# Kernel tuning notes

Hardware: AMD Instinct MI355X
Metric: run time of the kernel (lower is better)

Reference implementation:

```python
import jax, jax.numpy as jnp
import numpy as np
from jax.experimental.ode import odeint

LATENT, HIDDEN, OUT, BATCH, T = 128, 256, 128, 4096, 100
DEC_H = 64  # MLPDecoder default hidden_dim


def setup_inputs() -> dict:
    key = jax.random.key(0)
    ks = jax.random.split(key, 8)
    s = lambda k, shp, fan: jax.random.normal(k, shp, jnp.float32) / np.sqrt(fan)
    return {
        "z0": jax.random.normal(ks[0], (BATCH, LATENT), jnp.float32),
        "times": jnp.arange(T, dtype=jnp.float32) * 0.01,  # increasing time grid
        # ode_func: tanh MLP latent->hidden->latent
        "W1": s(ks[1], (LATENT, HIDDEN), LATENT),
        "b1": jnp.zeros((HIDDEN,), jnp.float32),
        "W2": s(ks[2], (HIDDEN, LATENT), HIDDEN),
        "b2": jnp.zeros((LATENT,), jnp.float32),
        # MLPDecoder: latent->64->relu->64->relu->out
        "dW1": s(ks[3], (LATENT, DEC_H), LATENT),
        "db1": jnp.zeros((DEC_H,), jnp.float32),
        "dW2": s(ks[4], (DEC_H, DEC_H), DEC_H),
        "db2": jnp.zeros((DEC_H,), jnp.float32),
        "dW3": s(ks[5], (DEC_H, OUT), DEC_H),
        "db3": jnp.zeros((OUT,), jnp.float32),
    }


def reference(z0, times, W1, b1, W2, b2, dW1, db1, dW2, db2, dW3, db3):
    def ode_func(z, t):  # dz/dt, autonomous tanh-MLP dynamics
        return jnp.tanh(z @ W1 + b1) @ W2 + b2

    # adaptive dopri5 (Dormand-Prince RK45), tolerances match torchdiffeq defaults
    z_traj = odeint(ode_func, z0, times, rtol=1e-7, atol=1e-9)  # [T, B, L]

    h = jax.nn.relu(z_traj @ dW1 + db1)
    h = jax.nn.relu(h @ dW2 + db2)
    y = h @ dW3 + db3                  # [T, B, out]
    return jnp.transpose(y, (1, 0, 2))  # [B, T, out]
```

## Files before the change

kernel.cpp:

```cpp
#include <hip/hip_runtime.h>

#define LATENT 128
#define HIDDEN 256
#define OUTD   128
#define TT     100
#define DECH   64
#define NMACRO 5

typedef _Float16 f16x8 __attribute__((ext_vector_type(8)));
typedef float    f32x4 __attribute__((ext_vector_type(4)));

#define MFMA16(a,b,c) __builtin_amdgcn_mfma_f32_16x16x32_f16((a),(b),(c),0,0,0)

__device__ __forceinline__ float tanh_fast(float x){
    float e = __expf(2.f*x);
    return 1.f - 2.f*__builtin_amdgcn_rcpf(e + 1.f);
}

__device__ __forceinline__ void bar_nodrain(){
    __builtin_amdgcn_sched_barrier(0);
    asm volatile("s_waitcnt lgkmcnt(0)" ::: "memory");
    __builtin_amdgcn_sched_barrier(0);
    __builtin_amdgcn_s_barrier();
    __builtin_amdgcn_sched_barrier(0);
}

__device__ __forceinline__ f16x8 lds_rd8(const _Float16* b, int sB, int row, int colE){
    int off = row*sB + colE*2; off ^= (row&7)<<4;
    return *(const f16x8*)((const char*)b + off);
}
__device__ __forceinline__ void lds_wr1(_Float16* b, int sB, int row, int colE, float v){
    int off = row*sB + colE*2; off ^= (row&7)<<4;
    *(_Float16*)((char*)b + off) = (_Float16)v;
}
__device__ __forceinline__ void lds_wr2(_Float16* b, int sB, int row, int colE, float lo, float hi){
    int off = row*sB + colE*2; off ^= (row&7)<<4;
    union { _Float16 h[2]; unsigned u; } pk;
    pk.h[0] = (_Float16)lo; pk.h[1] = (_Float16)hi;
    *(unsigned*)((char*)b + off) = pk.u;
}

__device__ __forceinline__ f16x8 gbl_bfrag(const float* W, int ldN, int k0, int n){
    f16x8 f;
#pragma unroll
    for(int i=0;i<8;++i) f[i] = (_Float16)W[(size_t)(k0+i)*ldN + n];
    return f;
}
__device__ __forceinline__ f16x8 gbl_bfrag_pk(const float* W, int ldN, int q, int lg, int n){
    f16x8 f;
#pragma unroll
    for(int i=0;i<8;++i){
        int k = 32*q + 4*lg + (i>>1) + 16*(i&1);
        f[i] = (_Float16)W[(size_t)k*ldN + n];
    }
    return f;
}

__global__ __launch_bounds__(512, 2) void ode_decoder_kernel(
    const float* __restrict__ z0, const float* __restrict__ times,
    const float* __restrict__ W1, const float* __restrict__ b1,
    const float* __restrict__ W2, const float* __restrict__ b2,
    const float* __restrict__ dW1, const float* __restrict__ db1,
    const float* __restrict__ dW2, const float* __restrict__ db2,
    const float* __restrict__ dW3, const float* __restrict__ db3,
    float* __restrict__ out)
{
    __shared__ _Float16 z_lds[16*LATENT]  __attribute__((aligned(16)));
    __shared__ _Float16 h_lds[16*HIDDEN]  __attribute__((aligned(16)));
    __shared__ _Float16 epz[16*LATENT]    __attribute__((aligned(16)));
    __shared__ _Float16 epf[16*LATENT]    __attribute__((aligned(16)));
    __shared__ _Float16 h1i[2][64*DECH]   __attribute__((aligned(16)));
    __shared__ _Float16 h2i[2][64*DECH]   __attribute__((aligned(16)));
    __shared__ float    tl[TT];

    const int tid  = threadIdx.x;
    const int wv   = tid >> 6;
    const int lane = tid & 63;
    const int lr   = lane & 15;
    const int lg   = lane >> 4;
    const int row0 = 4*lg;
    const int gRow0 = blockIdx.x * 16;
    const int nsl  = wv & 3;
    const int mtb  = 2*(wv >> 2);
    const int ph   = wv >> 2;

    if(tid < TT) tl[tid] = times[tid];

    f16x8 w1f[2][4];
#pragma unroll
    for(int t=0;t<2;++t)
#pragma unroll
        for(int q=0;q<4;++q)
            w1f[t][q] = gbl_bfrag(W1, HIDDEN, 32*q+8*lg, 32*wv+16*t+lr);
    f16x8 w2f[8];
#pragma unroll
    for(int q=0;q<8;++q)
        w2f[q] = gbl_bfrag_pk(W2, LATENT, q, lg, 16*wv+lr);

    f16x8 dw1f[4], dw2f[2], dw3f[2];
#pragma unroll
    for(int q=0;q<4;++q) dw1f[q] = gbl_bfrag(dW1, DECH, 32*q+8*lg, 16*nsl+lr);
#pragma unroll
    for(int q=0;q<2;++q) dw2f[q] = gbl_bfrag(dW2, DECH, 32*q+8*lg, 16*nsl+lr);
#pragma unroll
    for(int q=0;q<2;++q) dw3f[q] = gbl_bfrag(dW3, OUTD, 32*q+8*lg, 16*wv+lr);

    const float b1v0 = b1[32*wv+lr], b1v1 = b1[32*wv+16+lr];
    const float b2v  = b2[16*wv+lr];
    const float db1v = db1[16*nsl+lr], db2v = db2[16*nsl+lr];
    const float db3v = db3[16*wv+lr];

    f32x4 z, acc = {0,0,0,0};
    f32x4 UA = {0,0,0,0}, VA = {0,0,0,0}, UB = {0,0,0,0}, VB = {0,0,0,0};
#pragma unroll
    for(int r=0;r<4;++r){
        z[r] = z0[(size_t)(gRow0+row0+r)*LATENT + 16*wv + lr];
        lds_wr1(z_lds, LATENT*2, row0+r, 16*wv+lr, z[r]);
    }
    bar_nodrain();

    auto G1SEG = [&]{
        f16x8 az[4];
#pragma unroll
        for(int q=0;q<4;++q) az[q] = lds_rd8(z_lds, LATENT*2, lr, 32*q+8*lg);
        f32x4 c0 = {b1v0,b1v0,b1v0,b1v0};
        f32x4 c1 = {b1v1,b1v1,b1v1,b1v1};
#pragma unroll
        for(int q=0;q<4;++q){ c0 = MFMA16(az[q], w1f[0][q], c0); c1 = MFMA16(az[q], w1f[1][q], c1); }
#pragma unroll
        for(int r=0;r<4;++r)
            lds_wr2(h_lds, HIDDEN*2, row0+r, 2*(16*wv+lr), tanh_fast(c0[r]), tanh_fast(c1[r]));
    };
    auto G2SEG = [&]() -> f32x4 {
        f16x8 ah[8];
#pragma unroll
        for(int q=0;q<8;++q) ah[q] = lds_rd8(h_lds, HIDDEN*2, lr, 32*q+8*lg);
        f32x4 ca = {b2v,b2v,b2v,b2v}, cb = {0,0,0,0};
#pragma unroll
        for(int q=0;q<4;++q){ ca = MFMA16(ah[q], w2f[q], ca); cb = MFMA16(ah[4+q], w2f[4+q], cb); }
        return ca + cb;
    };
    auto WRZ = [&](f32x4 zs){
#pragma unroll
        for(int r=0;r<4;++r) lds_wr1(z_lds, LATENT*2, row0+r, 16*wv+lr, zs[r]);
    };
    auto WREP = [&](f32x4 zz, f32x4 ff){
#pragma unroll
        for(int r=0;r<4;++r){
            lds_wr1(epz, LATENT*2, row0+r, 16*wv+lr, zz[r]);
            lds_wr1(epf, LATENT*2, row0+r, 16*wv+lr, ff[r]);
        }
    };
    auto UVGEMM = [&]{
        f32x4 u = {0,0,0,0}, v = {0,0,0,0};
#pragma unroll
        for(int q=0;q<4;++q){
            u = MFMA16(lds_rd8(epz, LATENT*2, lr, 32*q+8*lg), dw1f[q], u);
            v = MFMA16(lds_rd8(epf, LATENT*2, lr, 32*q+8*lg), dw1f[q], v);
        }
        UB = u; VB = v;
    };
    auto CMB = [&](int par, int p0, int jj){
        const float t0 = tl[20*jj];
        const float tB = (jj==NMACRO-1) ? tl[TT-1] : tl[20*jj+20];
        const float hp = tB - t0, rhp = 1.f/hp;
        _Float16* h1 = h1i[par];
#pragma unroll
        for(int i=0;i<2;++i){
            const int pi = 2*ph + i;
            const float th = (tl[p0+pi]-t0)*rhp;
            const float t2 = th*th, t3 = t2*th;
            const float a0 = 2.f*t3-3.f*t2+1.f, a1 = (t3-2.f*t2+th)*hp;
            const float a2 = 3.f*t2-2.f*t3,     a3 = (t3-t2)*hp;
#pragma unroll
            for(int r=0;r<4;++r){
                float v = a0*UA[r] + a1*VA[r] + a2*UB[r] + a3*VB[r] + db1v;
                lds_wr1(h1, DECH*2, 16*pi+row0+r, 16*nsl+lr, fmaxf(v,0.f));
            }
        }
    };
    auto DG2 = [&](int par){
        const _Float16* h1 = h1i[par];
        _Float16* h2 = h2i[par];
#pragma unroll
        for(int m=0;m<2;++m){ int mt = mtb+m;
            f32x4 c = {db2v,db2v,db2v,db2v};
#pragma unroll
            for(int q=0;q<2;++q) c = MFMA16(lds_rd8(h1, DECH*2, 16*mt+lr, 32*q+8*lg), dw2f[q], c);
#pragma unroll
            for(int r=0;r<4;++r) lds_wr1(h2, DECH*2, 16*mt+row0+r, 16*nsl+lr, fmaxf(c[r],0.f));
        }
    };
    auto DG3 = [&](int par, int p0){
        const _Float16* h2 = h2i[par];
#pragma unroll
        for(int mt=0;mt<4;++mt){
            f32x4 c = {db3v,db3v,db3v,db3v};
#pragma unroll
            for(int q=0;q<2;++q) c = MFMA16(lds_rd8(h2, DECH*2, 16*mt+lr, 32*q+8*lg), dw3f[q], c);
#pragma unroll
            for(int r=0;r<4;++r)
                out[(size_t)(gRow0+row0+r)*TT*OUTD + (size_t)(p0+mt)*OUTD + 16*wv+lr] = c[r];
        }
    };

#pragma unroll 1
    for(int j=0;j<NMACRO;++j){
        const int  m0 = 20*j;
        const int  m1 = (m0+20 < TT-1) ? m0+20 : TT-1;
        const float hj = tl[m1]-tl[m0];
        const bool dA = (j>=1);
        const bool dD = (j>=2);
        const int  rb = 5*(j-1);

        G1SEG(); if(dD){ DG2((rb-1)&1); DG3((rb-2)&1, 4*(rb-2)); }
        bar_nodrain();
        {
            f32x4 k1 = G2SEG();
            WREP(z, k1);
            if(dD) DG3((rb-1)&1, 4*(rb-1));
            acc = z + k1*(hj*(1.f/6.f));
            WRZ(z + k1*(hj*0.5f));
        }
        bar_nodrain();
        G1SEG(); UVGEMM();
        bar_nodrain();
        {
            f32x4 k2 = G2SEG();
            if(dA) CMB(rb&1, 4*rb, j-1);
            acc += k2*(hj*(1.f/3.f));
            WRZ(z + k2*(hj*0.5f));
        }
        bar_nodrain();
        G1SEG(); if(dA){ CMB((rb+1)&1, 4*(rb+1), j-1); DG2(rb&1); }
        bar_nodrain();
        {
            f32x4 k3 = G2SEG();
            if(dA){ CMB((rb+2)&1, 4*(rb+2), j-1); DG2((rb+1)&1); DG3(rb&1, 4*rb); }
            acc += k3*(hj*(1.f/3.f));
            WRZ(z + k3*hj);
        }
        bar_nodrain();
        G1SEG(); if(dA){ CMB((rb+3)&1, 4*(rb+3), j-1); DG2((rb+2)&1); DG3((rb+1)&1, 4*(rb+1)); }
        bar_nodrain();
        {
            f32x4 k4 = G2SEG();
            if(dA){ CMB((rb+4)&1, 4*(rb+4), j-1); DG2((rb+3)&1); DG3((rb+2)&1, 4*(rb+2)); }
            z = acc + k4*(hj*(1.f/6.f));
            WRZ(z);
        }
        UA = UB; VA = VB;
        bar_nodrain();
    }

    {
        G1SEG(); DG2(19&1); DG3(18&1, 72);
        bar_nodrain();
        {
            f32x4 kt = G2SEG();
            WREP(z, kt);
            DG3(19&1, 76);
        }
        bar_nodrain();
        UVGEMM();
        bar_nodrain();
        CMB(20&1, 80, 4);
        bar_nodrain();
        CMB(21&1, 84, 4); DG2(20&1);
        bar_nodrain();
        CMB(22&1, 88, 4); DG2(21&1); DG3(20&1, 80);
        bar_nodrain();
        CMB(23&1, 92, 4); DG2(22&1); DG3(21&1, 84);
        bar_nodrain();
        CMB(24&1, 96, 4); DG2(23&1); DG3(22&1, 88);
        bar_nodrain();
        DG2(24&1); DG3(23&1, 92);
        bar_nodrain();
        DG3(24&1, 96);
    }
}

extern "C" void kernel_launch(void* const* d_in, const int* in_sizes, int n_in,
                              void* d_out, int out_size, void* d_ws, size_t ws_size,
                              hipStream_t stream) {
    ode_decoder_kernel<<<dim3(256), dim3(512), 0, stream>>>(
        (const float*)d_in[0],  (const float*)d_in[1],
        (const float*)d_in[2],  (const float*)d_in[3],
        (const float*)d_in[4],  (const float*)d_in[5],
        (const float*)d_in[6],  (const float*)d_in[7],
        (const float*)d_in[8],  (const float*)d_in[9],
        (const float*)d_in[10], (const float*)d_in[11],
        (float*)d_out);
}
```

Before: 59.40 us.

## Specialize waves into ODE-solver and decoder groups with double-buffered endpoint LDS

```diff
diff --git a/kernel.cpp b/kernel.cpp
--- a/kernel.cpp
+++ b/kernel.cpp
@@ -56,7 +56,7 @@
     return f;
 }
 
-__global__ __launch_bounds__(512, 2) void ode_decoder_kernel(
+__global__ __launch_bounds__(512, 1) void ode_decoder_kernel(
     const float* __restrict__ z0, const float* __restrict__ times,
     const float* __restrict__ W1, const float* __restrict__ b1,
     const float* __restrict__ W2, const float* __restrict__ b2,
@@ -65,12 +65,12 @@
     const float* __restrict__ dW3, const float* __restrict__ db3,
     float* __restrict__ out)
 {
-    __shared__ _Float16 z_lds[16*LATENT]  __attribute__((aligned(16)));
-    __shared__ _Float16 h_lds[16*HIDDEN]  __attribute__((aligned(16)));
-    __shared__ _Float16 epz[16*LATENT]    __attribute__((aligned(16)));
-    __shared__ _Float16 epf[16*LATENT]    __attribute__((aligned(16)));
-    __shared__ _Float16 h1i[2][64*DECH]   __attribute__((aligned(16)));
-    __shared__ _Float16 h2i[2][64*DECH]   __attribute__((aligned(16)));
+    __shared__ _Float16 z_lds[16*LATENT]   __attribute__((aligned(16)));
+    __shared__ _Float16 h_lds[16*HIDDEN]   __attribute__((aligned(16)));
+    __shared__ _Float16 epz[2][16*LATENT]  __attribute__((aligned(16)));
+    __shared__ _Float16 epf[2][16*LATENT]  __attribute__((aligned(16)));
+    __shared__ _Float16 h1i[2][64*DECH]    __attribute__((aligned(16)));
+    __shared__ _Float16 h2i[2][64*DECH]    __attribute__((aligned(16)));
     __shared__ float    tl[TT];
 
     const int tid  = threadIdx.x;
@@ -80,42 +80,55 @@
     const int lg   = lane >> 4;
     const int row0 = 4*lg;
     const int gRow0 = blockIdx.x * 16;
-    const int nsl  = wv & 3;
-    const int mtb  = 2*(wv >> 2);
-    const int ph   = wv >> 2;
+    const bool ct  = (wv < 4);
+    const int wc   = wv & 3;
+    const int dwv  = wv & 3;
+    const int nsl  = dwv;
 
     if(tid < TT) tl[tid] = times[tid];
 
-    f16x8 w1f[2][4];
-#pragma unroll
-    for(int t=0;t<2;++t)
-#pragma unroll
-        for(int q=0;q<4;++q)
-            w1f[t][q] = gbl_bfrag(W1, HIDDEN, 32*q+8*lg, 32*wv+16*t+lr);
-    f16x8 w2f[8];
-#pragma unroll
-    for(int q=0;q<8;++q)
-        w2f[q] = gbl_bfrag_pk(W2, LATENT, q, lg, 16*wv+lr);
-
-    f16x8 dw1f[4], dw2f[2], dw3f[2];
-#pragma unroll
-    for(int q=0;q<4;++q) dw1f[q] = gbl_bfrag(dW1, DECH, 32*q+8*lg, 16*nsl+lr);
-#pragma unroll
-    for(int q=0;q<2;++q) dw2f[q] = gbl_bfrag(dW2, DECH, 32*q+8*lg, 16*nsl+lr);
-#pragma unroll
-    for(int q=0;q<2;++q) dw3f[q] = gbl_bfrag(dW3, OUTD, 32*q+8*lg, 16*wv+lr);
-
-    const float b1v0 = b1[32*wv+lr], b1v1 = b1[32*wv+16+lr];
-    const float b2v  = b2[16*wv+lr];
-    const float db1v = db1[16*nsl+lr], db2v = db2[16*nsl+lr];
-    const float db3v = db3[16*wv+lr];
-
-    f32x4 z, acc = {0,0,0,0};
+    f16x8 w1f[4][4], w2f[2][8];
+    f32x4 z[2], acc[2];
+    float b1v[4], b2v[2];
+    f16x8 dw1f[4], dw2f[2], dw3f[2][2];
     f32x4 UA = {0,0,0,0}, VA = {0,0,0,0}, UB = {0,0,0,0}, VB = {0,0,0,0};
-#pragma unroll
-    for(int r=0;r<4;++r){
-        z[r] = z0[(size_t)(gRow0+row0+r)*LATENT + 16*wv + lr];
-        lds_wr1(z_lds, LATENT*2, row0+r, 16*wv+lr, z[r]);
+    float db1v = 0.f, db2v = 0.f, db3v[2] = {0.f,0.f};
+
+    if(ct){
+#pragma unroll
+        for(int t=0;t<4;++t)
+#pragma unroll
+            for(int q=0;q<4;++q)
+                w1f[t][q] = gbl_bfrag(W1, HIDDEN, 32*q+8*lg, 64*wc+16*t+lr);
+#pragma unroll
+        for(int u=0;u<2;++u)
+#pragma unroll
+            for(int q=0;q<8;++q)
+                w2f[u][q] = gbl_bfrag_pk(W2, LATENT, q, lg, 32*wc+16*u+lr);
+#pragma unroll
+        for(int t=0;t<4;++t) b1v[t] = b1[64*wc+16*t+lr];
+#pragma unroll
+        for(int u=0;u<2;++u) b2v[u] = b2[32*wc+16*u+lr];
+#pragma unroll
+        for(int u=0;u<2;++u)
+#pragma unroll
+            for(int r=0;r<4;++r){
+                z[u][r] = z0[(size_t)(gRow0+row0+r)*LATENT + 32*wc+16*u+lr];
+                lds_wr1(z_lds, LATENT*2, row0+r, 32*wc+16*u+lr, z[u][r]);
+            }
+    } else {
+#pragma unroll
+        for(int q=0;q<4;++q) dw1f[q] = gbl_bfrag(dW1, DECH, 32*q+8*lg, 16*nsl+lr);
+#pragma unroll
+        for(int q=0;q<2;++q) dw2f[q] = gbl_bfrag(dW2, DECH, 32*q+8*lg, 16*nsl+lr);
+#pragma unroll
+        for(int u=0;u<2;++u)
+#pragma unroll
+            for(int q=0;q<2;++q)
+                dw3f[u][q] = gbl_bfrag(dW3, OUTD, 32*q+8*lg, 32*dwv+16*u+lr);
+        db1v = db1[16*nsl+lr]; db2v = db2[16*nsl+lr];
+#pragma unroll
+        for(int u=0;u<2;++u) db3v[u] = db3[32*dwv+16*u+lr];
     }
     bar_nodrain();
 
@@ -123,40 +136,58 @@
         f16x8 az[4];
 #pragma unroll
         for(int q=0;q<4;++q) az[q] = lds_rd8(z_lds, LATENT*2, lr, 32*q+8*lg);
-        f32x4 c0 = {b1v0,b1v0,b1v0,b1v0};
-        f32x4 c1 = {b1v1,b1v1,b1v1,b1v1};
-#pragma unroll
-        for(int q=0;q<4;++q){ c0 = MFMA16(az[q], w1f[0][q], c0); c1 = MFMA16(az[q], w1f[1][q], c1); }
-#pragma unroll
-        for(int r=0;r<4;++r)
-            lds_wr2(h_lds, HIDDEN*2, row0+r, 2*(16*wv+lr), tanh_fast(c0[r]), tanh_fast(c1[r]));
-    };
-    auto G2SEG = [&]() -> f32x4 {
+        f32x4 c[4];
+#pragma unroll
+        for(int t=0;t<4;++t) c[t] = (f32x4){b1v[t],b1v[t],b1v[t],b1v[t]};
+#pragma unroll
+        for(int q=0;q<4;++q)
+#pragma unroll
+            for(int t=0;t<4;++t) c[t] = MFMA16(az[q], w1f[t][q], c[t]);
+#pragma unroll
+        for(int m=0;m<2;++m){
+            const int uu = 2*wc+m;
+#pragma unroll
+            for(int r=0;r<4;++r)
+                lds_wr2(h_lds, HIDDEN*2, row0+r, 2*(16*uu+lr),
+                        tanh_fast(c[2*m][r]), tanh_fast(c[2*m+1][r]));
+        }
+    };
+    auto G2SEG = [&](f32x4 kk[2]){
         f16x8 ah[8];
 #pragma unroll
         for(int q=0;q<8;++q) ah[q] = lds_rd8(h_lds, HIDDEN*2, lr, 32*q+8*lg);
-        f32x4 ca = {b2v,b2v,b2v,b2v}, cb = {0,0,0,0};
-#pragma unroll
-        for(int q=0;q<4;++q){ ca = MFMA16(ah[q], w2f[q], ca); cb = MFMA16(ah[4+q], w2f[4+q], cb); }
-        return ca + cb;
-    };
-    auto WRZ = [&](f32x4 zs){
-#pragma unroll
-        for(int r=0;r<4;++r) lds_wr1(z_lds, LATENT*2, row0+r, 16*wv+lr, zs[r]);
-    };
-    auto WREP = [&](f32x4 zz, f32x4 ff){
+#pragma unroll
+        for(int u=0;u<2;++u){
+            f32x4 ca = (f32x4){b2v[u],b2v[u],b2v[u],b2v[u]};
+            f32x4 cb = (f32x4){0,0,0,0};
+#pragma unroll
+            for(int q=0;q<4;++q){ ca = MFMA16(ah[q], w2f[u][q], ca); cb = MFMA16(ah[4+q], w2f[u][4+q], cb); }
+            kk[u] = ca + cb;
+        }
+    };
+    auto WRZ = [&](f32x4 zs0, f32x4 zs1){
 #pragma unroll
         for(int r=0;r<4;++r){
-            lds_wr1(epz, LATENT*2, row0+r, 16*wv+lr, zz[r]);
-            lds_wr1(epf, LATENT*2, row0+r, 16*wv+lr, ff[r]);
-        }
-    };
-    auto UVGEMM = [&]{
+            lds_wr1(z_lds, LATENT*2, row0+r, 32*wc+lr,    zs0[r]);
+            lds_wr1(z_lds, LATENT*2, row0+r, 32*wc+16+lr, zs1[r]);
+        }
+    };
+    auto WREP = [&](int par, f32x4 kk[2]){
+#pragma unroll
+        for(int u=0;u<2;++u)
+#pragma unroll
+            for(int r=0;r<4;++r){
+                lds_wr1(epz[par], LATENT*2, row0+r, 32*wc+16*u+lr, z[u][r]);
+                lds_wr1(epf[par], LATENT*2, row0+r, 32*wc+16*u+lr, kk[u][r]);
+            }
+    };
+
+    auto UVGEMM = [&](int par){
         f32x4 u = {0,0,0,0}, v = {0,0,0,0};
 #pragma unroll
         for(int q=0;q<4;++q){
-            u = MFMA16(lds_rd8(epz, LATENT*2, lr, 32*q+8*lg), dw1f[q], u);
-            v = MFMA16(lds_rd8(epf, LATENT*2, lr, 32*q+8*lg), dw1f[q], v);
+            u = MFMA16(lds_rd8(epz[par], LATENT*2, lr, 32*q+8*lg), dw1f[q], u);
+            v = MFMA16(lds_rd8(epf[par], LATENT*2, lr, 32*q+8*lg), dw1f[q], v);
         }
         UB = u; VB = v;
     };
@@ -166,8 +197,7 @@
         const float hp = tB - t0, rhp = 1.f/hp;
         _Float16* h1 = h1i[par];
 #pragma unroll
-        for(int i=0;i<2;++i){
-            const int pi = 2*ph + i;
+        for(int pi=0;pi<4;++pi){
             const float th = (tl[p0+pi]-t0)*rhp;
             const float t2 = th*th, t3 = t2*th;
             const float a0 = 2.f*t3-3.f*t2+1.f, a1 = (t3-2.f*t2+th)*hp;
@@ -183,7 +213,7 @@
         const _Float16* h1 = h1i[par];
         _Float16* h2 = h2i[par];
 #pragma unroll
-        for(int m=0;m<2;++m){ int mt = mtb+m;
+        for(int mt=0;mt<4;++mt){
             f32x4 c = {db2v,db2v,db2v,db2v};
 #pragma unroll
             for(int q=0;q<2;++q) c = MFMA16(lds_rd8(h1, DECH*2, 16*mt+lr, 32*q+8*lg), dw2f[q], c);
@@ -195,12 +225,18 @@
         const _Float16* h2 = h2i[par];
 #pragma unroll
         for(int mt=0;mt<4;++mt){
-            f32x4 c = {db3v,db3v,db3v,db3v};
-#pragma unroll
-            for(int q=0;q<2;++q) c = MFMA16(lds_rd8(h2, DECH*2, 16*mt+lr, 32*q+8*lg), dw3f[q], c);
-#pragma unroll
-            for(int r=0;r<4;++r)
-                out[(size_t)(gRow0+row0+r)*TT*OUTD + (size_t)(p0+mt)*OUTD + 16*wv+lr] = c[r];
+            f16x8 a[2];
+#pragma unroll
+            for(int q=0;q<2;++q) a[q] = lds_rd8(h2, DECH*2, 16*mt+lr, 32*q+8*lg);
+#pragma unroll
+            for(int u=0;u<2;++u){
+                f32x4 c = {db3v[u],db3v[u],db3v[u],db3v[u]};
+#pragma unroll
+                for(int q=0;q<2;++q) c = MFMA16(a[q], dw3f[u][q], c);
+#pragma unroll
+                for(int r=0;r<4;++r)
+                    out[(size_t)(gRow0+row0+r)*TT*OUTD + (size_t)(p0+mt)*OUTD + 32*dwv+16*u+lr] = c[r];
+            }
         }
     };
 
@@ -212,71 +248,72 @@
         const bool dA = (j>=1);
         const bool dD = (j>=2);
         const int  rb = 5*(j-1);
-
-        G1SEG(); if(dD){ DG2((rb-1)&1); DG3((rb-2)&1, 4*(rb-2)); }
-        bar_nodrain();
-        {
-            f32x4 k1 = G2SEG();
-            WREP(z, k1);
-            if(dD) DG3((rb-1)&1, 4*(rb-1));
-            acc = z + k1*(hj*(1.f/6.f));
-            WRZ(z + k1*(hj*0.5f));
-        }
-        bar_nodrain();
-        G1SEG(); UVGEMM();
-        bar_nodrain();
-        {
-            f32x4 k2 = G2SEG();
-            if(dA) CMB(rb&1, 4*rb, j-1);
-            acc += k2*(hj*(1.f/3.f));
-            WRZ(z + k2*(hj*0.5f));
-        }
-        bar_nodrain();
-        G1SEG(); if(dA){ CMB((rb+1)&1, 4*(rb+1), j-1); DG2(rb&1); }
-        bar_nodrain();
-        {
-            f32x4 k3 = G2SEG();
-            if(dA){ CMB((rb+2)&1, 4*(rb+2), j-1); DG2((rb+1)&1); DG3(rb&1, 4*rb); }
-            acc += k3*(hj*(1.f/3.f));
-            WRZ(z + k3*hj);
-        }
-        bar_nodrain();
-        G1SEG(); if(dA){ CMB((rb+3)&1, 4*(rb+3), j-1); DG2((rb+2)&1); DG3((rb+1)&1, 4*(rb+1)); }
-        bar_nodrain();
-        {
-            f32x4 k4 = G2SEG();
+        f32x4 kk[2];
+
+        if(ct) G1SEG(); else if(dD){ DG2((rb-1)&1); DG3((rb-2)&1, 4*(rb-2)); }
+        bar_nodrain();
+        if(ct){
+            G2SEG(kk);
+            WREP(j&1, kk);
+#pragma unroll
+            for(int u=0;u<2;++u) acc[u] = z[u] + kk[u]*(hj*(1.f/6.f));
+            WRZ(z[0] + kk[0]*(hj*0.5f), z[1] + kk[1]*(hj*0.5f));
+        } else if(dD) DG3((rb-1)&1, 4*(rb-1));
+        bar_nodrain();
+        if(ct) G1SEG(); else UVGEMM(j&1);
+        bar_nodrain();
+        if(ct){
+            G2SEG(kk);
+#pragma unroll
+            for(int u=0;u<2;++u) acc[u] += kk[u]*(hj*(1.f/3.f));
+            WRZ(z[0] + kk[0]*(hj*0.5f), z[1] + kk[1]*(hj*0.5f));
+        } else if(dA) CMB(rb&1, 4*rb, j-1);
+        bar_nodrain();
+        if(ct) G1SEG(); else if(dA){ CMB((rb+1)&1, 4*(rb+1), j-1); DG2(rb&1); }
+        bar_nodrain();
+        if(ct){
+            G2SEG(kk);
+#pragma unroll
+            for(int u=0;u<2;++u) acc[u] += kk[u]*(hj*(1.f/3.f));
+            WRZ(z[0] + kk[0]*hj, z[1] + kk[1]*hj);
+        } else if(dA){ CMB((rb+2)&1, 4*(rb+2), j-1); DG2((rb+1)&1); DG3(rb&1, 4*rb); }
+        bar_nodrain();
+        if(ct) G1SEG(); else if(dA){ CMB((rb+3)&1, 4*(rb+3), j-1); DG2((rb+2)&1); DG3((rb+1)&1, 4*(rb+1)); }
+        bar_nodrain();
+        if(ct){
+            G2SEG(kk);
+#pragma unroll
+            for(int u=0;u<2;++u) z[u] = acc[u] + kk[u]*(hj*(1.f/6.f));
+            WRZ(z[0], z[1]);
+        } else {
             if(dA){ CMB((rb+4)&1, 4*(rb+4), j-1); DG2((rb+3)&1); DG3((rb+2)&1, 4*(rb+2)); }
-            z = acc + k4*(hj*(1.f/6.f));
-            WRZ(z);
-        }
-        UA = UB; VA = VB;
+            UA = UB; VA = VB;
+        }
         bar_nodrain();
     }
 
     {
-        G1SEG(); DG2(19&1); DG3(18&1, 72);
-        bar_nodrain();
-        {
-            f32x4 kt = G2SEG();
-            WREP(z, kt);
-            DG3(19&1, 76);
-        }
-        bar_nodrain();
-        UVGEMM();
-        bar_nodrain();
-        CMB(20&1, 80, 4);
-        bar_nodrain();
-        CMB(21&1, 84, 4); DG2(20&1);
-        bar_nodrain();
-        CMB(22&1, 88, 4); DG2(21&1); DG3(20&1, 80);
-        bar_nodrain();
-        CMB(23&1, 92, 4); DG2(22&1); DG3(21&1, 84);
-        bar_nodrain();
-        CMB(24&1, 96, 4); DG2(23&1); DG3(22&1, 88);
-        bar_nodrain();
-        DG2(24&1); DG3(23&1, 92);
-        bar_nodrain();
-        DG3(24&1, 96);
+        f32x4 kk[2];
+        if(ct) G1SEG(); else { DG2(19&1); DG3(18&1, 72); }
+        bar_nodrain();
+        if(ct){ G2SEG(kk); WREP(NMACRO&1, kk); }
+        else DG3(19&1, 76);
+        bar_nodrain();
+        if(!ct) UVGEMM(NMACRO&1);
+        bar_nodrain();
+        if(!ct) CMB(20&1, 80, 4);
+        bar_nodrain();
+        if(!ct){ CMB(21&1, 84, 4); DG2(20&1); }
+        bar_nodrain();
+        if(!ct){ CMB(22&1, 88, 4); DG2(21&1); DG3(20&1, 80); }
+        bar_nodrain();
+        if(!ct){ CMB(23&1, 92, 4); DG2(22&1); DG3(21&1, 84); }
+        bar_nodrain();
+        if(!ct){ CMB(24&1, 96, 4); DG2(23&1); DG3(22&1, 88); }
+        bar_nodrain();
+        if(!ct){ DG2(24&1); DG3(23&1, 92); }
+        bar_nodrain();
+        if(!ct) DG3(24&1, 96);
     }
 }
 
```

Result: slower. 145.2 us (+144.4%).
